# Optimization experiments

Measured on AMD Instinct MI355X. Metric: run time of the kernel, lower is better.

Reference implementation:

```python
import jax, jax.numpy as jnp
import numpy as np
import math

B, S, H, HKV, DH = 2, 2048, 32, 1, 128  # batch, seq, q heads, kv heads, per-head/model dim
D_K = 128


def setup_inputs() -> dict:
    key = jax.random.key(0)
    ks = jax.random.split(key, 11)
    sc = 0.02
    return {
        "query": jax.random.normal(ks[0], (B, S, DH), jnp.float32),
        "key": jax.random.normal(ks[1], (B, S, DH), jnp.float32),
        "values": jax.random.normal(ks[2], (B, S, DH), jnp.float32),
        "W_q": jax.random.normal(ks[3], (DH, H * DH), jnp.float32) * sc,
        "b_q": jnp.zeros((H * DH,), jnp.float32),
        "W_k": jax.random.normal(ks[4], (DH, HKV * DH), jnp.float32) * sc,
        "b_k": jnp.zeros((HKV * DH,), jnp.float32),
        "W_v": jax.random.normal(ks[5], (DH, HKV * DH), jnp.float32) * sc,
        "b_v": jnp.zeros((HKV * DH,), jnp.float32),
        "W_o": jax.random.normal(ks[6], (H * DH, DH), jnp.float32) * sc,
        "b_o": jnp.zeros((DH,), jnp.float32),
    }


def reference(query, key, values, W_q, b_q, W_k, b_k, W_v, b_v, W_o, b_o):
    # Projections (note: the original uses raw .view(-1, H, S, DH), which we
    # replicate exactly — it is a reshape, not a transpose).
    q = (query @ W_q + b_q).reshape(-1, H, S, DH)      # [B,H,S,DH]
    k = (key @ W_k + b_k).reshape(-1, HKV, S, DH)       # [B,1,S,DH]
    v = (values @ W_v + b_v).reshape(-1, HKV, S, DH)    # [B,1,S,DH]

    # RoPE outputs in the original forward are computed but never used
    # (dead code), and mask defaults to None -> no masking. Dropout omitted
    # for deterministic reference.
    scores = jnp.matmul(q, jnp.swapaxes(k, -1, -2)) / math.sqrt(D_K)  # [B,H,S,S]
    attn = jax.nn.softmax(scores, axis=-1)
    out = jnp.matmul(attn, v)                           # [B,H,S,DH]
    out = jnp.swapaxes(out, 1, 2).reshape(-1, S, H * DH)
    return out @ W_o + b_o                              # [B,S,DH]
```

## Files before the change

kernel.cpp:

```cpp
#include <hip/hip_runtime.h>
#include <hip/hip_bf16.h>
#include <math.h>


typedef __hip_bfloat16 bf16;
typedef __attribute__((ext_vector_type(8))) short short8;
typedef __attribute__((ext_vector_type(4))) float floatx4;

static constexpr int B_ = 2;
static constexpr int S_ = 2048;
static constexpr int H_ = 32;
static constexpr int DH_ = 128;

#define GL16(gp, lp)                                              \
  __builtin_amdgcn_global_load_lds(                               \
      (const __attribute__((address_space(1))) void*)(gp),        \
      (__attribute__((address_space(3))) void*)(lp), 16, 0, 0)

static __device__ __forceinline__ unsigned bpack(float lo, float hi) {
  unsigned a = __float_as_uint(lo) + 0x8000u;
  unsigned b = __float_as_uint(hi) + 0x8000u;
  return __builtin_amdgcn_perm(b, a, 0x07060302u);
}

static __device__ __forceinline__ bool detect_f32(
    const unsigned short* __restrict__ q) {
  int t = threadIdx.x & 63;
  int cnt = 0;
#pragma unroll
  for (int i = 0; i < 8; ++i) {
    unsigned short u = q[t * 8 + i];
    int e = (u >> 7) & 0xFF;
    if (e < 0x60) cnt++;
  }
#pragma unroll
  for (int off = 1; off < 64; off <<= 1) cnt += __shfl_xor(cnt, off);
  return cnt >= 8;
}

static __device__ __forceinline__ short8 loadA8(const void* __restrict__ base,
                                                size_t elt, bool f) {
  if (f) {
    const float4* p = (const float4*)((const float*)base + elt);
    float4 x = p[0], y = p[1];
    union { unsigned u[4]; short8 v; } r;
    r.u[0] = bpack(x.x, x.y);
    r.u[1] = bpack(x.z, x.w);
    r.u[2] = bpack(y.x, y.y);
    r.u[3] = bpack(y.z, y.w);
    return r.v;
  }
  return *(const short8*)((const bf16*)base + elt);
}

static __device__ void do_ttranspose(const void* __restrict__ W,
                                     bf16* __restrict__ Wt, int K, int N,
                                     bool f, float scale, int bx, int by,
                                     bf16 (*tile)[66]) {
  int n0 = bx * 64, k0 = by * 64;
  int c = threadIdx.x & 63;
  int r4 = threadIdx.x >> 6;
#pragma unroll
  for (int i = 0; i < 16; ++i) {
    int r = r4 * 16 + i;
    float v = f ? ((const float*)W)[(size_t)(k0 + r) * N + n0 + c]
                : __bfloat162float(((const bf16*)W)[(size_t)(k0 + r) * N + n0 + c]);
    tile[r][c] = __float2bfloat16(v * scale);
  }
  __syncthreads();
#pragma unroll
  for (int i = 0; i < 16; ++i) {
    int cc = r4 * 16 + i;
    Wt[(size_t)(n0 + cc) * K + k0 + c] = tile[c][cc];
  }
}

__global__ __launch_bounds__(256) void gemm_qkv(
    const void* __restrict__ query, const void* __restrict__ key,
    const void* __restrict__ values, const void* __restrict__ Wq,
    const void* __restrict__ Wk, const void* __restrict__ Wv,
    const void* __restrict__ Wo, const void* __restrict__ bq,
    const void* __restrict__ bk, const void* __restrict__ bv,
    bf16* __restrict__ Qp, bf16* __restrict__ Kp, bf16* __restrict__ Vtp,
    bf16* __restrict__ Wot, float qscale) {
  __shared__ __align__(16) bf16 sh[64 * 136];
  const bool f = detect_f32((const unsigned short*)query);
  const int bx = blockIdx.x;
  const int yb = blockIdx.y;

  if (bx >= 68) {
    int j = (bx - 68) * 8 + yb;
    do_ttranspose(Wo, Wot, H_ * DH_, DH_, f, 1.0f, j % 2, j / 2,
                  (bf16(*)[66])sh);
    return;
  }

  const void* A; const void* W; const void* bias; bf16* Cb;
  int mode, ldc, colb, N; float wsc, bsc;
  if (bx < 64)      { A = query;  W = Wq; bias = bq; Cb = Qp;  mode = 0; ldc = 4096; colb = bx;      N = 4096; wsc = qscale; bsc = qscale; }
  else if (bx < 66) { A = key;    W = Wk; bias = bk; Cb = Kp;  mode = 0; ldc = 128;  colb = bx - 64; N = 128;  wsc = 1.f;    bsc = 1.f; }
  else              { A = values; W = Wv; bias = bv; Cb = Vtp; mode = 3; ldc = 0;    colb = bx - 66; N = 128;  wsc = 1.f;    bsc = 1.f; }
  const int col_base = colb * 64;

  {
    int c = threadIdx.x & 63, r4 = threadIdx.x >> 6;
#pragma unroll
    for (int i = 0; i < 32; ++i) {
      int k = r4 * 32 + i;
      float v = f ? ((const float*)W)[(size_t)k * N + col_base + c]
                  : __bfloat162float(
                        ((const bf16*)W)[(size_t)k * N + col_base + c]);
      sh[c * 136 + k] = __float2bfloat16(v * wsc);
    }
  }

  const int lane = threadIdx.x & 63;
  const int wave = threadIdx.x >> 6;
  const int lm = lane & 15;
  const int quad = lane >> 4;

  float bt[4];
#pragma unroll
  for (int t = 0; t < 4; ++t) {
    int col = col_base + t * 16 + lm;
    float v = f ? ((const float*)bias)[col]
                : __bfloat162float(((const bf16*)bias)[col]);
    bt[t] = v * bsc;
  }
  __syncthreads();

  floatx4 z = {0.f, 0.f, 0.f, 0.f};
#pragma unroll
  for (int rt = 0; rt < 8; ++rt) {
    const int row_base = (yb * 8 + rt) * 64 + wave * 16;
    const size_t aelt = (size_t)(row_base + lm) * DH_ + quad * 8;
    floatx4 acc[4] = {z, z, z, z};
#pragma unroll
    for (int kk = 0; kk < DH_; kk += 32) {
      short8 a = loadA8(A, aelt + kk, f);
#pragma unroll
      for (int t = 0; t < 4; ++t) {
        short8 b = *(const short8*)(&sh[(t * 16 + lm) * 136 + quad * 8 + kk]);
        acc[t] = __builtin_amdgcn_mfma_f32_16x16x32_bf16(a, b, acc[t], 0, 0, 0);
      }
    }
#pragma unroll
    for (int t = 0; t < 4; ++t) {
      int col = col_base + t * 16 + lm;
#pragma unroll
      for (int r = 0; r < 4; ++r) {
        int row = row_base + quad * 4 + r;
        if (mode == 0) {
          Cb[(size_t)row * ldc + col] = __float2bfloat16(acc[t][r] + bt[t]);
        } else {
          Cb[((size_t)((row >> 11) * DH_ + col)) * S_ + (row & 2047)] =
              __float2bfloat16(acc[t][r] + bt[t]);
        }
      }
    }
  }
}

__global__ __launch_bounds__(256) void gemm_out(
    const bf16* __restrict__ A, const bf16* __restrict__ Bt,
    float* __restrict__ Cf) {
  constexpr int K_len = (H_ * DH_) / 16;
  const int lane = threadIdx.x & 63;
  const int wave = threadIdx.x >> 6;
  const int lm = lane & 15;
  const int quad = lane >> 4;
  const int row_base = blockIdx.x * 64 + wave * 16;
  const int koff = blockIdx.y * K_len;

  const bf16* arow = A + (size_t)(row_base + lm) * (H_ * DH_) + koff + quad * 8;
  const bf16* brow = Bt + (size_t)lm * (H_ * DH_) + koff + quad * 8;

  floatx4 z = {0.f, 0.f, 0.f, 0.f};
  floatx4 acc[8] = {z, z, z, z, z, z, z, z};
#pragma unroll 2
  for (int kk = 0; kk < K_len; kk += 32) {
    short8 a = *(const short8*)(arow + kk);
#pragma unroll
    for (int t = 0; t < 8; ++t) {
      short8 b = *(const short8*)(brow + (size_t)(t * 16) * (H_ * DH_) + kk);
      acc[t] = __builtin_amdgcn_mfma_f32_16x16x32_bf16(a, b, acc[t], 0, 0, 0);
    }
  }
#pragma unroll
  for (int t = 0; t < 8; ++t) {
    int col = t * 16 + lm;
#pragma unroll
    for (int r = 0; r < 4; ++r) {
      int row = row_base + quad * 4 + r;
      Cf[(size_t)blockIdx.y * (4096 * 128) + (size_t)row * DH_ + col] =
          acc[t][r];
    }
  }
}

__global__ void finish_out(const float* __restrict__ parts,
                           const void* __restrict__ bo_raw,
                           const unsigned short* __restrict__ qdet,
                           float* __restrict__ out) {
  const bool f = detect_f32(qdet);
  int i = blockIdx.x * 256 + threadIdx.x;
  const float4* p = (const float4*)parts;
  float4 o;
  int cb = (i & 31) * 4;
  if (f) {
    o = ((const float4*)bo_raw)[i & 31];
  } else {
    const bf16* bb = (const bf16*)bo_raw;
    o.x = __bfloat162float(bb[cb + 0]);
    o.y = __bfloat162float(bb[cb + 1]);
    o.z = __bfloat162float(bb[cb + 2]);
    o.w = __bfloat162float(bb[cb + 3]);
  }
#pragma unroll
  for (int j = 0; j < 16; ++j) {
    float4 a = p[i + (size_t)j * 131072];
    o.x += a.x; o.y += a.y; o.z += a.z; o.w += a.w;
  }
  ((float4*)out)[i] = o;
}

static __device__ __forceinline__ float fexp2(float x) {
#if __has_builtin(__builtin_amdgcn_exp2f)
  return __builtin_amdgcn_exp2f(x);
#else
  return exp2f(x);
#endif
}

static __device__ __forceinline__ void pexchange(const unsigned pk[8],
                                                 int quad, short8* pf) {
  const bool q0 = (quad & 1);
  unsigned sA0 = q0 ? pk[0] : pk[2];
  unsigned sA1 = q0 ? pk[1] : pk[3];
  unsigned sA2 = q0 ? pk[4] : pk[6];
  unsigned sA3 = q0 ? pk[5] : pk[7];
  unsigned r0 = (unsigned)__shfl_xor((int)sA0, 16);
  unsigned r1 = (unsigned)__shfl_xor((int)sA1, 16);
  unsigned r2 = (unsigned)__shfl_xor((int)sA2, 16);
  unsigned r3 = (unsigned)__shfl_xor((int)sA3, 16);
  unsigned M0 = q0 ? r0 : pk[0];
  unsigned M1 = q0 ? r1 : pk[1];
  unsigned M2 = q0 ? pk[2] : r0;
  unsigned M3 = q0 ? pk[3] : r1;
  unsigned M4 = q0 ? r2 : pk[4];
  unsigned M5 = q0 ? r3 : pk[5];
  unsigned M6 = q0 ? pk[6] : r2;
  unsigned M7 = q0 ? pk[7] : r3;
  const bool swp = (quad == 1) || (quad == 2);
  union { unsigned u[4]; short8 v; } f0, f1;
  unsigned t0, t1;
  t0 = (unsigned)__shfl_xor((int)M0, 48); f0.u[0] = swp ? t0 : M0;
  t1 = (unsigned)__shfl_xor((int)M1, 48); f0.u[1] = swp ? t1 : M1;
  t0 = (unsigned)__shfl_xor((int)M2, 48); f0.u[2] = swp ? t0 : M2;
  t1 = (unsigned)__shfl_xor((int)M3, 48); f0.u[3] = swp ? t1 : M3;
  t0 = (unsigned)__shfl_xor((int)M4, 48); f1.u[0] = swp ? t0 : M4;
  t1 = (unsigned)__shfl_xor((int)M5, 48); f1.u[1] = swp ? t1 : M5;
  t0 = (unsigned)__shfl_xor((int)M6, 48); f1.u[2] = swp ? t0 : M6;
  t1 = (unsigned)__shfl_xor((int)M7, 48); f1.u[3] = swp ? t1 : M7;
  pf[0] = f0.v;
  pf[1] = f1.v;
}

__global__ __launch_bounds__(256, 2) void flash_attn(
    const bf16* __restrict__ Qp, const bf16* __restrict__ Kp,
    const bf16* __restrict__ Vt, bf16* __restrict__ O2c) {
  const int tid = threadIdx.x;
  const int lane = tid & 63;
  const int wave = tid >> 6;
  const int lm = lane & 15;
  const int quad = lane >> 4;
  const int qt = blockIdx.x;
  const int h = blockIdx.y;
  const int b = blockIdx.z;

  __shared__ __align__(16) bf16 Klds[64 * 128];
  __shared__ __align__(16) bf16 Vlds[2][128 * 64];

  const int base = qt * 128 + wave * 32;
  const bf16* qrow = Qp + ((size_t)b * S_ + h * 64 + (base >> 5)) * 4096;
  short8 qf0[4], qf1[4];
#pragma unroll
  for (int ks = 0; ks < 4; ++ks) {
    qf0[ks] = *(const short8*)(qrow + lm * 128 + quad * 8 + ks * 32);
    qf1[ks] = *(const short8*)(qrow + (16 + lm) * 128 + quad * 8 + ks * 32);
  }

  const bf16* Kb = Kp + (size_t)b * S_ * DH_;
  const bf16* Vb = Vt + (size_t)b * DH_ * S_;
  const int sw = lm & 7;

  const bf16* kgp[4];
  const bf16* vgp[4];
#pragma unroll
  for (int i = 0; i < 4; ++i) {
    const int inst = wave * 4 + i;
    const int krow = inst * 4 + quad;
    kgp[i] = Kb + (size_t)krow * 128 + ((lm ^ (krow & 7)) * 8);
    const int vrow = inst * 8 + (lane >> 3);
    vgp[i] = Vb + (size_t)vrow * S_ + (((lane & 7) ^ (vrow & 7)) * 8);
  }

  floatx4 z = {0.f, 0.f, 0.f, 0.f};
  floatx4 oa0[8], oa1[8];
#pragma unroll
  for (int nt = 0; nt < 8; ++nt) { oa0[nt] = z; oa1[nt] = z; }
  float ls0 = 0.f, ls1 = 0.f;

#pragma unroll
  for (int i = 0; i < 4; ++i) {
    GL16(kgp[i], &Klds[(wave * 4 + i) * 512]);
    GL16(vgp[i], &Vlds[0][(wave * 4 + i) * 512]);
    kgp[i] += 64 * 128;
    vgp[i] += 64;
  }

  int cur = 0;
  for (int kb = 0; kb < S_; kb += 64) {
    __syncthreads();
    const bool more = kb + 64 < S_;
    if (more) {
#pragma unroll
      for (int i = 0; i < 4; ++i) {
        GL16(vgp[i], &Vlds[cur ^ 1][(wave * 4 + i) * 512]);
        vgp[i] += 64;
      }
    }

    floatx4 s0[4] = {z, z, z, z}, s1[4] = {z, z, z, z};
    __builtin_amdgcn_s_setprio(1);
#pragma unroll
    for (int t = 0; t < 4; ++t) {
#pragma unroll
      for (int ks = 0; ks < 4; ++ks) {
        short8 kf = *(const short8*)(&Klds[(t * 16 + lm) * 128 +
                                           (((quad + 4 * ks) ^ sw) * 8)]);
        s0[t] = __builtin_amdgcn_mfma_f32_16x16x32_bf16(kf, qf0[ks], s0[t],
                                                        0, 0, 0);
        s1[t] = __builtin_amdgcn_mfma_f32_16x16x32_bf16(kf, qf1[ks], s1[t],
                                                        0, 0, 0);
      }
    }
    __builtin_amdgcn_s_setprio(0);

    __syncthreads();
    if (more) {
#pragma unroll
      for (int i = 0; i < 4; ++i) {
        GL16(kgp[i], &Klds[(wave * 4 + i) * 512]);
        kgp[i] += 64 * 128;
      }
    }

    unsigned pk0[8], pk1[8];
#pragma unroll
    for (int t = 0; t < 4; ++t) {
      float a0 = fexp2(s0[t][0]), a1 = fexp2(s0[t][1]);
      float a2 = fexp2(s0[t][2]), a3 = fexp2(s0[t][3]);
      ls0 += (a0 + a1) + (a2 + a3);
      pk0[2 * t] = bpack(a0, a1);
      pk0[2 * t + 1] = bpack(a2, a3);
      float c0 = fexp2(s1[t][0]), c1 = fexp2(s1[t][1]);
      float c2 = fexp2(s1[t][2]), c3 = fexp2(s1[t][3]);
      ls1 += (c0 + c1) + (c2 + c3);
      pk1[2 * t] = bpack(c0, c1);
      pk1[2 * t + 1] = bpack(c2, c3);
    }
    short8 pf0[2], pf1[2];
    pexchange(pk0, quad, pf0);
    pexchange(pk1, quad, pf1);

    __builtin_amdgcn_s_setprio(1);
#pragma unroll
    for (int ks2 = 0; ks2 < 2; ++ks2) {
#pragma unroll
      for (int nt = 0; nt < 8; ++nt) {
        short8 vf = *(const short8*)(&Vlds[cur][(nt * 16 + lm) * 64 +
                                              (((quad + 4 * ks2) ^ sw) * 8)]);
        oa0[nt] = __builtin_amdgcn_mfma_f32_16x16x32_bf16(pf0[ks2], vf,
                                                          oa0[nt], 0, 0, 0);
        oa1[nt] = __builtin_amdgcn_mfma_f32_16x16x32_bf16(pf1[ks2], vf,
                                                          oa1[nt], 0, 0, 0);
      }
    }
    __builtin_amdgcn_s_setprio(0);
    cur ^= 1;
  }

  ls0 += __shfl_xor(ls0, 16);
  ls0 += __shfl_xor(ls0, 32);
  ls1 += __shfl_xor(ls1, 16);
  ls1 += __shfl_xor(ls1, 32);
  float inv0[4], inv1[4];
#pragma unroll
  for (int r = 0; r < 4; ++r) {
    inv0[r] = 1.0f / __shfl(ls0, quad * 4 + r);
    inv1[r] = 1.0f / __shfl(ls1, quad * 4 + r);
  }

#pragma unroll
  for (int r = 0; r < 4; ++r) {
    int s2a = base + quad * 4 + r;
    int s2b = s2a + 16;
    size_t ba = ((size_t)b * S_ + s2a) * 4096 + (size_t)h * 128;
    size_t bb = ((size_t)b * S_ + s2b) * 4096 + (size_t)h * 128;
#pragma unroll
    for (int nt = 0; nt < 8; ++nt) {
      O2c[ba + nt * 16 + lm] = __float2bfloat16(oa0[nt][r] * inv0[r]);
      O2c[bb + nt * 16 + lm] = __float2bfloat16(oa1[nt][r] * inv1[r]);
    }
  }
}

extern "C" void kernel_launch(void* const* d_in, const int* in_sizes, int n_in,
                              void* d_out, int out_size, void* d_ws,
                              size_t ws_size, hipStream_t stream) {
  (void)in_sizes;
  (void)n_in;
  (void)out_size;
  (void)ws_size;

  const void* query = d_in[0];
  const void* key = d_in[1];
  const void* values = d_in[2];
  const void* W_q = d_in[3];
  const void* b_q = d_in[4];
  const void* W_k = d_in[5];
  const void* b_k = d_in[6];
  const void* W_v = d_in[7];
  const void* b_v = d_in[8];
  const void* W_o = d_in[9];
  const void* b_o = d_in[10];
  float* out = (float*)d_out;

  const float kScale = 0.1275174388204085f;
  const int M = B_ * S_;
  const int QN = B_ * S_ * DH_;

  char* w = (char*)d_ws;
  auto carve = [&](size_t bytes) -> char* {
    char* p = w;
    w += (bytes + 255) & ~(size_t)255;
    return p;
  };
  bf16* Wot = (bf16*)carve((size_t)H_ * DH_ * DH_ * 2);
  bf16* Kp = (bf16*)carve((size_t)B_ * S_ * DH_ * 2);
  bf16* Vtp = (bf16*)carve((size_t)B_ * S_ * DH_ * 2);
  bf16* Qp = (bf16*)carve((size_t)M * H_ * DH_ * 2);
  bf16* O2c = (bf16*)carve((size_t)M * H_ * DH_ * 2);

  float* parts = (float*)Qp;

  gemm_qkv<<<dim3(84, 8), 256, 0, stream>>>(query, key, values, W_q, W_k,
                                            W_v, W_o, b_q, b_k, b_v, Qp, Kp,
                                            Vtp, Wot, kScale);

  flash_attn<<<dim3(S_ / 128, H_, B_), 256, 0, stream>>>(Qp, Kp, Vtp, O2c);

  gemm_out<<<dim3(M / 64, 16), 256, 0, stream>>>(O2c, Wot, parts);

  finish_out<<<QN / 4 / 256, 256, 0, stream>>>(
      parts, b_o, (const unsigned short*)query, out);
}
```

Baseline: 310.2 us.

## Software-pipeline PV matmul with triple-buffered V and atomic split-K output

The attention loop now defers each block's P·V MFMAs to the next iteration, overlapping them with the next QK^T and softmax exponentials, which requires a third V buffer in LDS. Separately, the output projection now uses 8 K-splits that atomically add into an output buffer pre-initialized with the bias by a new kernel. This replaces the 16-way partial buffer and the separate reduction kernel. The extra LDS may reduce occupancy, and float atomics make the summation order nondeterministic.

```diff
diff --git a/kernel.cpp b/kernel.cpp
--- a/kernel.cpp
+++ b/kernel.cpp
@@ -73,6 +73,25 @@
     int cc = r4 * 16 + i;
     Wt[(size_t)(n0 + cc) * K + k0 + c] = tile[c][cc];
   }
+}
+
+__global__ void init_out(const void* __restrict__ bo_raw,
+                         const unsigned short* __restrict__ qdet,
+                         float* __restrict__ out) {
+  const bool f = detect_f32(qdet);
+  int i = blockIdx.x * 256 + threadIdx.x;
+  float4 o;
+  int cb = (i & 31) * 4;
+  if (f) {
+    o = ((const float4*)bo_raw)[i & 31];
+  } else {
+    const bf16* bb = (const bf16*)bo_raw;
+    o.x = __bfloat162float(bb[cb + 0]);
+    o.y = __bfloat162float(bb[cb + 1]);
+    o.z = __bfloat162float(bb[cb + 2]);
+    o.w = __bfloat162float(bb[cb + 3]);
+  }
+  ((float4*)out)[i] = o;
 }
 
 __global__ __launch_bounds__(256) void gemm_qkv(
@@ -163,8 +182,8 @@
 
 __global__ __launch_bounds__(256) void gemm_out(
     const bf16* __restrict__ A, const bf16* __restrict__ Bt,
-    float* __restrict__ Cf) {
-  constexpr int K_len = (H_ * DH_) / 16;
+    float* __restrict__ out) {
+  constexpr int K_len = (H_ * DH_) / 8;
   const int lane = threadIdx.x & 63;
   const int wave = threadIdx.x >> 6;
   const int lm = lane & 15;
@@ -192,36 +211,9 @@
 #pragma unroll
     for (int r = 0; r < 4; ++r) {
       int row = row_base + quad * 4 + r;
-      Cf[(size_t)blockIdx.y * (4096 * 128) + (size_t)row * DH_ + col] =
-          acc[t][r];
-    }
-  }
-}
-
-__global__ void finish_out(const float* __restrict__ parts,
-                           const void* __restrict__ bo_raw,
-                           const unsigned short* __restrict__ qdet,
-                           float* __restrict__ out) {
-  const bool f = detect_f32(qdet);
-  int i = blockIdx.x * 256 + threadIdx.x;
-  const float4* p = (const float4*)parts;
-  float4 o;
-  int cb = (i & 31) * 4;
-  if (f) {
-    o = ((const float4*)bo_raw)[i & 31];
-  } else {
-    const bf16* bb = (const bf16*)bo_raw;
-    o.x = __bfloat162float(bb[cb + 0]);
-    o.y = __bfloat162float(bb[cb + 1]);
-    o.z = __bfloat162float(bb[cb + 2]);
-    o.w = __bfloat162float(bb[cb + 3]);
-  }
-#pragma unroll
-  for (int j = 0; j < 16; ++j) {
-    float4 a = p[i + (size_t)j * 131072];
-    o.x += a.x; o.y += a.y; o.z += a.z; o.w += a.w;
-  }
-  ((float4*)out)[i] = o;
+      atomicAdd(&out[(size_t)row * DH_ + col], acc[t][r]);
+    }
+  }
 }
 
 static __device__ __forceinline__ float fexp2(float x) {
@@ -279,7 +271,7 @@
   const int b = blockIdx.z;
 
   __shared__ __align__(16) bf16 Klds[64 * 128];
-  __shared__ __align__(16) bf16 Vlds[2][128 * 64];
+  __shared__ __align__(16) bf16 Vlds[3][128 * 64];
 
   const int base = qt * 128 + wave * 32;
   const bf16* qrow = Qp + ((size_t)b * S_ + h * 64 + (base >> 5)) * 4096;
@@ -310,6 +302,7 @@
 #pragma unroll
   for (int nt = 0; nt < 8; ++nt) { oa0[nt] = z; oa1[nt] = z; }
   float ls0 = 0.f, ls1 = 0.f;
+  short8 pfp0[2], pfp1[2];
 
 #pragma unroll
   for (int i = 0; i < 4; ++i) {
@@ -319,14 +312,16 @@
     vgp[i] += 64;
   }
 
-  int cur = 0;
+  int vc = 0;
   for (int kb = 0; kb < S_; kb += 64) {
     __syncthreads();
     const bool more = kb + 64 < S_;
+    const int vnext = (vc == 2) ? 0 : vc + 1;
+    const int vprev = (vc == 0) ? 2 : vc - 1;
     if (more) {
 #pragma unroll
       for (int i = 0; i < 4; ++i) {
-        GL16(vgp[i], &Vlds[cur ^ 1][(wave * 4 + i) * 512]);
+        GL16(vgp[i], &Vlds[vnext][(wave * 4 + i) * 512]);
         vgp[i] += 64;
       }
     }
@@ -354,6 +349,23 @@
         GL16(kgp[i], &Klds[(wave * 4 + i) * 512]);
         kgp[i] += 64 * 128;
       }
+    }
+
+    if (kb > 0) {
+      __builtin_amdgcn_s_setprio(1);
+#pragma unroll
+      for (int ks2 = 0; ks2 < 2; ++ks2) {
+#pragma unroll
+        for (int nt = 0; nt < 8; ++nt) {
+          short8 vf = *(const short8*)(&Vlds[vprev][(nt * 16 + lm) * 64 +
+                                                    (((quad + 4 * ks2) ^ sw) * 8)]);
+          oa0[nt] = __builtin_amdgcn_mfma_f32_16x16x32_bf16(
+              ks2 ? pfp0[1] : pfp0[0], vf, oa0[nt], 0, 0, 0);
+          oa1[nt] = __builtin_amdgcn_mfma_f32_16x16x32_bf16(
+              ks2 ? pfp1[1] : pfp1[0], vf, oa1[nt], 0, 0, 0);
+        }
+      }
+      __builtin_amdgcn_s_setprio(0);
     }
 
     unsigned pk0[8], pk1[8];
@@ -373,22 +385,27 @@
     short8 pf0[2], pf1[2];
     pexchange(pk0, quad, pf0);
     pexchange(pk1, quad, pf1);
-
+    pfp0[0] = pf0[0]; pfp0[1] = pf0[1];
+    pfp1[0] = pf1[0]; pfp1[1] = pf1[1];
+    vc = vnext;
+  }
+
+  {
+    const int vlast = (vc == 0) ? 2 : vc - 1;
     __builtin_amdgcn_s_setprio(1);
 #pragma unroll
     for (int ks2 = 0; ks2 < 2; ++ks2) {
 #pragma unroll
       for (int nt = 0; nt < 8; ++nt) {
-        short8 vf = *(const short8*)(&Vlds[cur][(nt * 16 + lm) * 64 +
-                                              (((quad + 4 * ks2) ^ sw) * 8)]);
-        oa0[nt] = __builtin_amdgcn_mfma_f32_16x16x32_bf16(pf0[ks2], vf,
-                                                          oa0[nt], 0, 0, 0);
-        oa1[nt] = __builtin_amdgcn_mfma_f32_16x16x32_bf16(pf1[ks2], vf,
-                                                          oa1[nt], 0, 0, 0);
+        short8 vf = *(const short8*)(&Vlds[vlast][(nt * 16 + lm) * 64 +
+                                                  (((quad + 4 * ks2) ^ sw) * 8)]);
+        oa0[nt] = __builtin_amdgcn_mfma_f32_16x16x32_bf16(
+            ks2 ? pfp0[1] : pfp0[0], vf, oa0[nt], 0, 0, 0);
+        oa1[nt] = __builtin_amdgcn_mfma_f32_16x16x32_bf16(
+            ks2 ? pfp1[1] : pfp1[0], vf, oa1[nt], 0, 0, 0);
       }
     }
     __builtin_amdgcn_s_setprio(0);
-    cur ^= 1;
   }
 
   ls0 += __shfl_xor(ls0, 16);
@@ -453,7 +470,8 @@
   bf16* Qp = (bf16*)carve((size_t)M * H_ * DH_ * 2);
   bf16* O2c = (bf16*)carve((size_t)M * H_ * DH_ * 2);
 
-  float* parts = (float*)Qp;
+  init_out<<<QN / 4 / 256, 256, 0, stream>>>(
+      b_o, (const unsigned short*)query, out);
 
   gemm_qkv<<<dim3(84, 8), 256, 0, stream>>>(query, key, values, W_q, W_k,
                                             W_v, W_o, b_q, b_k, b_v, Qp, Kp,
@@ -461,8 +479,5 @@
 
   flash_attn<<<dim3(S_ / 128, H_, B_), 256, 0, stream>>>(Qp, Kp, Vtp, O2c);
 
-  gemm_out<<<dim3(M / 64, 16), 256, 0, stream>>>(O2c, Wot, parts);
-
-  finish_out<<<QN / 4 / 256, 256, 0, stream>>>(
-      parts, b_o, (const unsigned short*)query, out);
-}
+  gemm_out<<<dim3(M / 64, 8), 256, 0, stream>>>(O2c, Wot, out);
+}
```

Result: no change. 310.9 us (+0.2%).

## Replace split-K partial buffer and reduce kernel with atomic accumulation into output

Applied to the files above, without the earlier changes.

The output bias initialisation moves into extra blocks of the QKV projection kernel. The split-K output GEMM then atomically adds its partial tiles straight into the final output, so the separate finish_out reduction kernel and its 16-way partial buffer traffic are removed. The cost is contention from 16-way float atomics on every output element, plus a summation order that is no longer deterministic.

```diff
diff --git a/kernel.cpp b/kernel.cpp
--- a/kernel.cpp
+++ b/kernel.cpp
@@ -81,13 +81,31 @@
     const void* __restrict__ Wk, const void* __restrict__ Wv,
     const void* __restrict__ Wo, const void* __restrict__ bq,
     const void* __restrict__ bk, const void* __restrict__ bv,
-    bf16* __restrict__ Qp, bf16* __restrict__ Kp, bf16* __restrict__ Vtp,
-    bf16* __restrict__ Wot, float qscale) {
+    const void* __restrict__ bo, bf16* __restrict__ Qp,
+    bf16* __restrict__ Kp, bf16* __restrict__ Vtp, bf16* __restrict__ Wot,
+    float* __restrict__ out, float qscale) {
   __shared__ __align__(16) bf16 sh[64 * 136];
   const bool f = detect_f32((const unsigned short*)query);
   const int bx = blockIdx.x;
   const int yb = blockIdx.y;
 
+  if (bx >= 84) {
+    int j = (bx - 84) * 8 + yb;
+    int i = j * 256 + threadIdx.x;
+    float4 o;
+    int cb = (i & 31) * 4;
+    if (f) {
+      o = ((const float4*)bo)[i & 31];
+    } else {
+      const bf16* bb = (const bf16*)bo;
+      o.x = __bfloat162float(bb[cb + 0]);
+      o.y = __bfloat162float(bb[cb + 1]);
+      o.z = __bfloat162float(bb[cb + 2]);
+      o.w = __bfloat162float(bb[cb + 3]);
+    }
+    ((float4*)out)[i] = o;
+    return;
+  }
   if (bx >= 68) {
     int j = (bx - 68) * 8 + yb;
     do_ttranspose(Wo, Wot, H_ * DH_, DH_, f, 1.0f, j % 2, j / 2,
@@ -163,7 +181,7 @@
 
 __global__ __launch_bounds__(256) void gemm_out(
     const bf16* __restrict__ A, const bf16* __restrict__ Bt,
-    float* __restrict__ Cf) {
+    float* __restrict__ out) {
   constexpr int K_len = (H_ * DH_) / 16;
   const int lane = threadIdx.x & 63;
   const int wave = threadIdx.x >> 6;
@@ -192,36 +210,9 @@
 #pragma unroll
     for (int r = 0; r < 4; ++r) {
       int row = row_base + quad * 4 + r;
-      Cf[(size_t)blockIdx.y * (4096 * 128) + (size_t)row * DH_ + col] =
-          acc[t][r];
-    }
-  }
-}
-
-__global__ void finish_out(const float* __restrict__ parts,
-                           const void* __restrict__ bo_raw,
-                           const unsigned short* __restrict__ qdet,
-                           float* __restrict__ out) {
-  const bool f = detect_f32(qdet);
-  int i = blockIdx.x * 256 + threadIdx.x;
-  const float4* p = (const float4*)parts;
-  float4 o;
-  int cb = (i & 31) * 4;
-  if (f) {
-    o = ((const float4*)bo_raw)[i & 31];
-  } else {
-    const bf16* bb = (const bf16*)bo_raw;
-    o.x = __bfloat162float(bb[cb + 0]);
-    o.y = __bfloat162float(bb[cb + 1]);
-    o.z = __bfloat162float(bb[cb + 2]);
-    o.w = __bfloat162float(bb[cb + 3]);
-  }
-#pragma unroll
-  for (int j = 0; j < 16; ++j) {
-    float4 a = p[i + (size_t)j * 131072];
-    o.x += a.x; o.y += a.y; o.z += a.z; o.w += a.w;
-  }
-  ((float4*)out)[i] = o;
+      atomicAdd(&out[(size_t)row * DH_ + col], acc[t][r]);
+    }
+  }
 }
 
 static __device__ __forceinline__ float fexp2(float x) {
@@ -439,7 +430,6 @@
 
   const float kScale = 0.1275174388204085f;
   const int M = B_ * S_;
-  const int QN = B_ * S_ * DH_;
 
   char* w = (char*)d_ws;
   auto carve = [&](size_t bytes) -> char* {
@@ -453,16 +443,11 @@
   bf16* Qp = (bf16*)carve((size_t)M * H_ * DH_ * 2);
   bf16* O2c = (bf16*)carve((size_t)M * H_ * DH_ * 2);
 
-  float* parts = (float*)Qp;
-
-  gemm_qkv<<<dim3(84, 8), 256, 0, stream>>>(query, key, values, W_q, W_k,
-                                            W_v, W_o, b_q, b_k, b_v, Qp, Kp,
-                                            Vtp, Wot, kScale);
+  gemm_qkv<<<dim3(148, 8), 256, 0, stream>>>(query, key, values, W_q, W_k,
+                                             W_v, W_o, b_q, b_k, b_v, b_o,
+                                             Qp, Kp, Vtp, Wot, out, kScale);
 
   flash_attn<<<dim3(S_ / 128, H_, B_), 256, 0, stream>>>(Qp, Kp, Vtp, O2c);
 
-  gemm_out<<<dim3(M / 64, 16), 256, 0, stream>>>(O2c, Wot, parts);
-
-  finish_out<<<QN / 4 / 256, 256, 0, stream>>>(
-      parts, b_o, (const unsigned short*)query, out);
-}
+  gemm_out<<<dim3(M / 64, 16), 256, 0, stream>>>(O2c, Wot, out);
+}
```

After: 313.0 us. Within noise of the previous version (+0.9%).
